# Optimization experiments

Measured on AMD Instinct MI355X. Metric: run time of the kernel, lower is better.

Reference implementation:

```python
import jax, jax.numpy as jnp
import numpy as np

N_NODES = 20000
N_EDGES = 320000
F_IN = 64      # num_node_features
C = 64         # out_features (per-head channels, concat=False)
H = 4          # n_heads
L = 3          # n_layers (stackable since F_IN == C)
N_RES = 2
N_PAIRS = 8192
EDGE_DIM = 9
HID = 64 * C   # ResNetGated hidden dim = 64 * out_features
N_EXPERTS = 8


def setup_inputs() -> dict:
    key = jax.random.key(0)
    ks = jax.random.split(key, 24)
    s = 0.05
    f32 = jnp.float32
    inp = {}
    inp["x"] = jax.random.normal(ks[0], (N_NODES, F_IN), f32)
    inp["edge_index"] = jax.random.randint(ks[1], (2, N_EDGES), 0, N_NODES)
    inp["edge_attr"] = jax.random.normal(ks[2], (N_EDGES, EDGE_DIM), f32)
    inp["edge_cross"] = jax.random.randint(ks[3], (N_PAIRS, 2), 0, N_NODES)
    inp["types"] = jax.random.randint(ks[4], (N_PAIRS,), 0, N_EXPERTS)
    # GATv2 encoder params, stacked over L layers (layer 0 in-dim == C)
    inp["gat_Wl"] = jax.random.normal(ks[5], (L, F_IN, H * C), f32) * s
    inp["gat_bl"] = jnp.full((L, H * C), 0.01, f32)
    inp["gat_Wr"] = jax.random.normal(ks[6], (L, F_IN, H * C), f32) * s
    inp["gat_br"] = jnp.full((L, H * C), 0.01, f32)
    inp["gat_We"] = jax.random.normal(ks[7], (L, EDGE_DIM, H * C), f32) * s  # lin_edge, no bias
    inp["gat_att"] = jax.random.normal(ks[8], (L, H, C), f32) * s
    inp["gat_bias"] = jnp.zeros((L, C), f32)
    inp["gat_gates"] = jax.random.normal(ks[9], (L,), f32) * 0.5
    # 8 type-routed experts: ResNetGated(2C -> 64C -> 2C) x N_RES, then Linear(2C, 1)
    inp["res_W1"] = jax.random.normal(ks[10], (N_EXPERTS, N_RES, 2 * C, HID), f32) * s
    inp["res_b1"] = jnp.full((N_EXPERTS, N_RES, HID), 0.01, f32)
    inp["res_W2"] = jax.random.normal(ks[11], (N_EXPERTS, N_RES, HID, 2 * C), f32) * s
    inp["res_b2"] = jnp.full((N_EXPERTS, N_RES, 2 * C), 0.01, f32)
    inp["res_gates"] = jax.random.normal(ks[12], (N_EXPERTS, N_RES), f32) * 0.5
    inp["head_W"] = jax.random.normal(ks[13], (N_EXPERTS, 2 * C, 1), f32) * s
    inp["head_b"] = jnp.full((N_EXPERTS, 1), 0.01, f32)
    return inp


def _gat_layer(h, src, tgt, ea, Wl, bl, Wr, br, We, att, bias):
    # GATv2Conv with edge features, concat=False (mean over heads)
    n = h.shape[0]
    nh, c = att.shape
    xl = (h @ Wl + bl).reshape(n, nh, c)   # source transform (x_j)
    xr = (h @ Wr + br).reshape(n, nh, c)   # target transform (x_i)
    e = (ea @ We).reshape(-1, nh, c)
    m = jax.nn.leaky_relu(xl[src] + xr[tgt] + e, 0.2)       # [E,H,C]
    logits = jnp.einsum('ehc,hc->eh', m, att)               # [E,H]
    mx = jax.ops.segment_max(logits, tgt, num_segments=n)
    a = jnp.exp(logits - mx[tgt])
    den = jax.ops.segment_sum(a, tgt, num_segments=n)
    alpha = a / den[tgt]                                     # segment softmax over in-edges
    out = jax.ops.segment_sum(xl[src] * alpha[:, :, None], tgt, num_segments=n)
    return out.mean(axis=1) + bias


def reference(x, edge_index, edge_attr, edge_cross, types,
              gat_Wl, gat_bl, gat_Wr, gat_br, gat_We, gat_att, gat_bias, gat_gates,
              res_W1, res_b1, res_W2, res_b2, res_gates, head_W, head_b):
    src, tgt = edge_index[0], edge_index[1]
    g = jax.nn.sigmoid(gat_gates)
    h = _gat_layer(x, src, tgt, edge_attr, gat_Wl[0], gat_bl[0], gat_Wr[0], gat_br[0],
                   gat_We[0], gat_att[0], gat_bias[0])
    for i in range(1, gat_Wl.shape[0]):
        h = jax.nn.leaky_relu(h, 0.01)
        hi = _gat_layer(h, src, tgt, edge_attr, gat_Wl[i], gat_bl[i], gat_Wr[i], gat_br[i],
                        gat_We[i], gat_att[i], gat_bias[i])
        h = g[i - 1] * hi + (1 - g[i - 1]) * h
    # pair gather + feature interleave: x[edge_cross].transpose(1,2).reshape(P, 2C)
    pair = h[edge_cross]                               # [P,2,C]
    p = pair.shape[0]
    z0 = jnp.swapaxes(pair, 1, 2).reshape(p, -1)        # [P,2C]
    outs = []
    for e in range(res_W1.shape[0]):
        z = z0
        ge = jax.nn.sigmoid(res_gates[e])
        for r in range(res_W1.shape[1]):
            z = jax.nn.relu(z)
            y = jax.nn.relu(z @ res_W1[e, r] + res_b1[e, r]) @ res_W2[e, r] + res_b2[e, r]
            z = ge[r] * y + (1 - ge[r]) * z
        outs.append(z @ head_W[e] + head_b[e])          # [P,1]
    all_out = jnp.stack(outs)                           # [8,P,1]
    per_row = all_out[types, jnp.arange(p)]             # [P,1] per-row expert output
    order = jnp.argsort(types, stable=True)             # concat groups type 0..7, stable in-group
    return per_row[order]
```

## Files before the change

### kernel.cpp

```cpp
#include <hip/hip_runtime.h>

#define NN 20000
#define NE 320000
#define NL 3
#define NP 8192
#define EDIM 9
#define TROWS 32
#define MAXT 272
#define CAPR (MAXT*TROWS)
#define NB ((NN+255)/256)

typedef _Float16 f16x8 __attribute__((ext_vector_type(8)));
typedef float f32x4 __attribute__((ext_vector_type(4)));

#define GLL16(g,l) __builtin_amdgcn_global_load_lds((const __attribute__((address_space(1))) unsigned int*)(g), (__attribute__((address_space(3))) unsigned int*)(l), 16, 0, 0)

__device__ __forceinline__ float sigm(float x){ return 1.f/(1.f+__expf(-x)); }

__device__ __forceinline__ float dpp_sum64(float x){
  x += __int_as_float(__builtin_amdgcn_update_dpp(0, __float_as_int(x), 0x111, 0xf, 0xf, true));
  x += __int_as_float(__builtin_amdgcn_update_dpp(0, __float_as_int(x), 0x112, 0xf, 0xf, true));
  x += __int_as_float(__builtin_amdgcn_update_dpp(0, __float_as_int(x), 0x114, 0xf, 0xf, true));
  x += __int_as_float(__builtin_amdgcn_update_dpp(0, __float_as_int(x), 0x118, 0xf, 0xf, true));
  x += __int_as_float(__builtin_amdgcn_update_dpp(0, __float_as_int(x), 0x142, 0xf, 0xf, true));
  x += __int_as_float(__builtin_amdgcn_update_dpp(0, __float_as_int(x), 0x143, 0xf, 0xf, true));
  return __uint_as_float(__builtin_amdgcn_readlane(__float_as_uint(x), 63));
}

__global__ void k_deg(const int* __restrict__ ei, int* __restrict__ deg){
  int e=blockIdx.x*blockDim.x+threadIdx.x; if(e<NE) atomicAdd(&deg[ei[NE+e]],1);
}

__global__ __launch_bounds__(256) void k_scan1(const int* __restrict__ deg, int* __restrict__ incl, int* __restrict__ bsum){
  __shared__ int sh[256];
  int b=blockIdx.x, tid=threadIdx.x;
  int i=b*256+tid;
  int v=(i<NN)?deg[i]:0;
  sh[tid]=v; __syncthreads();
  for(int o=1;o<256;o<<=1){
    int t=(tid>=o)?sh[tid-o]:0; __syncthreads();
    sh[tid]+=t; __syncthreads();
  }
  if(i<NN) incl[i]=sh[tid];
  if(tid==255) bsum[b]=sh[255];
}
__global__ __launch_bounds__(256) void k_scan3(const int* __restrict__ deg, const int* __restrict__ incl,
                        const int* __restrict__ bsum, int* __restrict__ row_ptr, int* __restrict__ cursor){
  __shared__ int sh[256];
  int b=blockIdx.x, tid=threadIdx.x;
  sh[tid]=(tid<b && tid<NB)?bsum[tid]:0;
  __syncthreads();
  for(int o=128;o>0;o>>=1){ if(tid<o) sh[tid]+=sh[tid+o]; __syncthreads(); }
  int boff=sh[0];
  int i=b*256+tid;
  if(i<NN){
    int r=incl[i]+boff;
    row_ptr[i+1]=r; cursor[i]=r-deg[i];
  }
  if(i==0) row_ptr[0]=0;
}

__global__ void k_fill_csr2(const int* __restrict__ ei, const float* __restrict__ ea,
    int* __restrict__ cursor, int* __restrict__ csr_src, float* __restrict__ eas){
  int e=blockIdx.x*blockDim.x+threadIdx.x;
  if(e<NE){
    int t=ei[NE+e]; int pos=atomicAdd(&cursor[t],1);
    csr_src[pos]=ei[e];
    const float* s=ea+(size_t)e*9;
    float* d=eas+(size_t)pos*12;
    #pragma unroll
    for(int k=0;k<9;++k) d[k]=s[k];
    d[9]=0.f; d[10]=0.f; d[11]=0.f;
  }
}

__global__ __launch_bounds__(256) void k_sort(const int* __restrict__ types, int* __restrict__ meta,
    int* __restrict__ slotp, int* __restrict__ islot){
  __shared__ int cnt[256][8];
  __shared__ int tot[8];
  __shared__ int base_s[8], pad_s[8];
  int tid=threadIdx.x;
  int lc[8]={0,0,0,0,0,0,0,0};
  int tl[32];
  for(int i=0;i<32;++i){ int ty=types[tid*32+i]; tl[i]=ty; lc[ty]++; }
  #pragma unroll
  for(int t=0;t<8;++t) cnt[tid][t]=lc[t];
  __syncthreads();
  if(tid<8){
    int run=0;
    for(int j=0;j<256;++j){ int v=cnt[j][tid]; cnt[j][tid]=run; run+=v; }
    tot[tid]=run;
  }
  __syncthreads();
  if(tid==0){
    int b=0, pb=0, nt=0;
    for(int t=0;t<8;++t){
      base_s[t]=b; pad_s[t]=pb;
      meta[t]=tot[t]; meta[8+t]=b; meta[16+t]=pb;
      int ntt=(tot[t]+31)>>5;
      for(int j=0;j<ntt;++j){ meta[32+nt]=t; meta[32+MAXT+nt]=pb+j*32; nt++; }
      b+=tot[t]; pb+=ntt*32;
    }
    meta[24]=nt; meta[25]=pb;
  }
  __syncthreads();
  if(tid<8){
    int t=tid; int ntt=(tot[t]+31)>>5;
    for(int sr=tot[t]; sr<ntt*32; ++sr) islot[pad_s[t]+sr]=-1;
  }
  int run[8];
  #pragma unroll
  for(int t=0;t<8;++t) run[t]=cnt[tid][t];
  for(int i=0;i<32;++i){
    int p=tid*32+i; int t=tl[i]; int r=run[t]++;
    int pos=base_s[t]+r, slot=pad_s[t]+r;
    slotp[p]=slot; islot[slot]=pos;
  }
}

__global__ __launch_bounds__(256) void k_nodexf(const float* __restrict__ hin,
    const float* __restrict__ Wl, const float* __restrict__ bl,
    const float* __restrict__ Wr, const float* __restrict__ br,
    float* __restrict__ xl, float* __restrict__ xr, int lk){
  __shared__ float hsT[64][68];
  __shared__ float ws[64][68];
  int bid=blockIdx.x;
  int n0=(bid>>3)*64, ch=bid&7;
  const float* W=(ch<4)?Wl:Wr;
  const float* bb=(ch<4)?bl:br;
  float* outp=(ch<4)?xl:xr;
  int c0=(ch&3)*64;
  int tid=threadIdx.x;

  for(int idx=tid; idx<64*16; idx+=256){
    int r=idx&63, kq=idx>>6;
    int n=n0+r;
    float4 v=make_float4(0.f,0.f,0.f,0.f);
    if(n<NN) v=*(const float4*)&hin[(size_t)n*64+kq*4];
    if(lk){
      v.x=v.x>0.f?v.x:0.01f*v.x; v.y=v.y>0.f?v.y:0.01f*v.y;
      v.z=v.z>0.f?v.z:0.01f*v.z; v.w=v.w>0.f?v.w:0.01f*v.w;
    }
    hsT[kq*4+0][r]=v.x; hsT[kq*4+1][r]=v.y; hsT[kq*4+2][r]=v.z; hsT[kq*4+3][r]=v.w;
  }
  for(int idx=tid; idx<64*16; idx+=256){
    int k=idx>>4, j4=idx&15;
    *(float4*)&ws[k][j4*4]=*(const float4*)&W[(size_t)k*256+c0+j4*4];
  }
  __syncthreads();

  int ty=tid>>4, tx=tid&15;
  float acc[4][4]={};
  #pragma unroll 4
  for(int k=0;k<64;++k){
    float4 a=*(const float4*)&hsT[k][4*ty];
    float4 b=*(const float4*)&ws[k][4*tx];
    float aa[4]={a.x,a.y,a.z,a.w}, bbv[4]={b.x,b.y,b.z,b.w};
    #pragma unroll
    for(int i=0;i<4;++i){
      #pragma unroll
      for(int j=0;j<4;++j) acc[i][j]=fmaf(aa[i],bbv[j],acc[i][j]);
    }
  }
  float4 bias4=*(const float4*)&bb[c0+4*tx];
  #pragma unroll
  for(int i=0;i<4;++i){
    int n=n0+4*ty+i;
    if(n<NN){
      float4 o=make_float4(acc[i][0]+bias4.x, acc[i][1]+bias4.y, acc[i][2]+bias4.z, acc[i][3]+bias4.w);
      *(float4*)&outp[(size_t)n*256+c0+4*tx]=o;
    }
  }
}

__global__ __launch_bounds__(256) void k_agg2(const float* __restrict__ xl, const float* __restrict__ xr,
    const float* __restrict__ eas, const int* __restrict__ csr_src, const int* __restrict__ row_ptr,
    const float* __restrict__ WeL, const float* __restrict__ attL,
    const float* __restrict__ biasL, const float* __restrict__ gates, int layer,
    const float* __restrict__ hprev, float* __restrict__ hout){
  __shared__ float red[4][64];
  int n=blockIdx.x, tid=threadIdx.x;
  float w0=WeL[tid],      w1=WeL[256+tid],  w2=WeL[512+tid],  w3=WeL[768+tid],  w4=WeL[1024+tid];
  float w5=WeL[1280+tid], w6=WeL[1536+tid], w7=WeL[1792+tid], w8=WeL[2048+tid];
  float att_t=attL[tid];
  float xr_t=xr[(size_t)n*256+tid];
  int s=row_ptr[n], t=row_ptr[n+1];
  float den=0.f, acc=0.f;

  auto body=[&](float xlv, int j){
    const float4* ep=(const float4*)(eas+(size_t)j*12);
    float4 e0=ep[0], e1=ep[1];
    float e8=eas[(size_t)j*12+8];
    float ev=e0.x*w0+e0.y*w1+e0.z*w2+e0.w*w3+e1.x*w4+e1.y*w5+e1.z*w6+e1.w*w7+e8*w8;
    float m=xlv+xr_t+ev;
    m=m>0.f?m:0.2f*m;
    float pt=dpp_sum64(m*att_t);
    float a=__expf(pt);
    den+=a; acc+=a*xlv;
  };

  float x0=0.f,x1=0.f,x2=0.f,x3=0.f;
  if(s+0<t) x0=xl[(size_t)csr_src[s+0]*256+tid];
  if(s+1<t) x1=xl[(size_t)csr_src[s+1]*256+tid];
  if(s+2<t) x2=xl[(size_t)csr_src[s+2]*256+tid];
  if(s+3<t) x3=xl[(size_t)csr_src[s+3]*256+tid];
  int j=s;
  while(j+7<t){
    float y0=xl[(size_t)csr_src[j+4]*256+tid];
    float y1=xl[(size_t)csr_src[j+5]*256+tid];
    float y2=xl[(size_t)csr_src[j+6]*256+tid];
    float y3=xl[(size_t)csr_src[j+7]*256+tid];
    body(x0,j); body(x1,j+1); body(x2,j+2); body(x3,j+3);
    x0=y0; x1=y1; x2=y2; x3=y3;
    j+=4;
  }
  if(j<t){ body(x0,j); ++j; }
  if(j<t){ body(x1,j); ++j; }
  if(j<t){ body(x2,j); ++j; }
  if(j<t){ body(x3,j); ++j; }
  while(j<t){ body(xl[(size_t)csr_src[j]*256+tid], j); ++j; }

  float rdn=den>0.f?1.f/den:0.f;
  int h=tid>>6, cc=tid&63;
  red[h][cc]=acc*rdn;
  __syncthreads();
  if(tid<64){
    float mean=(red[0][tid]+red[1][tid]+red[2][tid]+red[3][tid])*0.25f + biasL[tid];
    float o;
    if(layer==0) o=mean;
    else{
      float hp=hprev[(size_t)n*64+tid];
      hp=hp>0.f?hp:0.01f*hp;
      float g=sigm(gates[layer-1]);
      o=g*mean+(1.f-g)*hp;
    }
    hout[(size_t)n*64+tid]=o;
  }
}

__global__ __launch_bounds__(256) void k_prep_all(const float* __restrict__ rW1, _Float16* __restrict__ w1t,
    const float* __restrict__ rW2, _Float16* __restrict__ w2t,
    const float* __restrict__ hfin, const int* __restrict__ ecross,
    const int* __restrict__ slotp, float* __restrict__ z){
  __shared__ float lds[128*33];
  int bigbid=blockIdx.x, tid=threadIdx.x;
  if(bigbid<2048){
    int bid=bigbid, er=bid>>7, ch=bid&127;
    const float* s=rW1+(size_t)er*128*4096 + ch*32;
    for(int idx=tid; idx<128*32; idx+=256){ int k=idx>>5, jl=idx&31; lds[k*33+jl]=s[(size_t)k*4096+jl]; }
    __syncthreads();
    _Float16* d=w1t+(size_t)bid*4096;
    for(int g=tid; g<512; g+=256){
      int jl=g>>4, k8=g&15;
      f16x8 v;
      #pragma unroll
      for(int t=0;t<8;++t) v[t]=(_Float16)lds[(k8*8+t)*33+jl];
      int elem=(jl*128+k8*8)^((jl&7)<<3);
      *(f16x8*)(&d[elem])=v;
    }
  }else if(bigbid<4096){
    int bid=bigbid-2048, er=bid>>7, ch=bid&127;
    const float* s=rW2+(size_t)er*4096*128 + (size_t)ch*32*128;
    for(int idx=tid; idx<32*128; idx+=256){ int j=idx>>7, n=idx&127; lds[j*130+n]=s[(size_t)j*128+n]; }
    __syncthreads();
    _Float16* d=w2t+(size_t)bid*4096;
    for(int g=tid; g<512; g+=256){
      int n=g>>2, j8=g&3;
      f16x8 v;
      #pragma unroll
      for(int t=0;t<8;++t) v[t]=(_Float16)lds[(j8*8+t)*130+n];
      int elem=(n*32+j8*8)^((n&7)<<3);
      *(f16x8*)(&d[elem])=v;
    }
  }else{
    int g=(bigbid-4096)*256+tid;
    int p=g>>6, c=g&63;
    int a=ecross[2*p], b=ecross[2*p+1];
    int slot=slotp[p];
    float2 v; v.x=hfin[(size_t)a*64+c]; v.y=hfin[(size_t)b*64+c];
    ((float2*)(z+(size_t)slot*128))[c]=v;
  }
}

__global__ __launch_bounds__(256) void k_resmfma(const float* __restrict__ zin,
    const _Float16* __restrict__ w1t, const _Float16* __restrict__ w2t,
    const float* __restrict__ b1all, const int* __restrict__ meta,
    float* __restrict__ ypart, int rb)
{
  __shared__ _Float16 zh[32*128];
  __shared__ _Float16 wb[3][8192];
  __shared__ _Float16 ts[2][32*32];
  __shared__ float b1s[1024];
  int bidl=blockIdx.x;
  int bid=(bidl&7)*132+(bidl>>3);
  int v=bid>>2, hq=bid&3;
  int nt=meta[24];
  if(v>=nt) return;
  int e=meta[32+v], row0=meta[32+MAXT+v];
  int er=e*2+rb;
  const _Float16* w1b=w1t+(size_t)er*524288 + (size_t)hq*32*4096;
  const _Float16* w2b=w2t+(size_t)er*524288 + (size_t)hq*32*4096;
  const float* b1g=b1all+(size_t)er*4096 + hq*1024;
  int tid=threadIdx.x, l=tid&63, w=tid>>6;
  int lm=l&15, lq=l>>4;
  int s16=(w&1)*16, jh=w>>1;
  int arow=s16+lm;

  for(int g=tid; g<512; g+=256){
    int row=g>>4, slot=g&15;
    const float* src=zin+(size_t)(row0+row)*128+slot*8;
    float4 v0=*(const float4*)src;
    float4 v1=*(const float4*)(src+4);
    f16x8 hv;
    hv[0]=(_Float16)fmaxf(v0.x,0.f); hv[1]=(_Float16)fmaxf(v0.y,0.f);
    hv[2]=(_Float16)fmaxf(v0.z,0.f); hv[3]=(_Float16)fmaxf(v0.w,0.f);
    hv[4]=(_Float16)fmaxf(v1.x,0.f); hv[5]=(_Float16)fmaxf(v1.y,0.f);
    hv[6]=(_Float16)fmaxf(v1.z,0.f); hv[7]=(_Float16)fmaxf(v1.w,0.f);
    *(f16x8*)(&zh[(row*128+slot*8)^((row&7)<<3)])=hv;
  }
  for(int g=tid; g<1024; g+=256) b1s[g]=b1g[g];

  #pragma unroll
  for(int s=0;s<2;++s){
    int so=(w*2+s)*512;
    GLL16(w1b+so+l*8, &wb[0][so]);
    GLL16(w2b+so+l*8, &wb[0][4096+so]);
  }
  {
    const _Float16* g1=w1b+4096;
    const _Float16* g2=w2b+4096;
    #pragma unroll
    for(int s=0;s<2;++s){
      int so=(w*2+s)*512;
      GLL16(g1+so+l*8, &wb[1][so]);
      GLL16(g2+so+l*8, &wb[1][4096+so]);
    }
  }
  asm volatile("s_waitcnt lgkmcnt(0)" ::: "memory");
  __builtin_amdgcn_sched_barrier(0);
  __builtin_amdgcn_s_barrier();

  f32x4 yacc[4];
  #pragma unroll
  for(int i=0;i<4;++i){ yacc[i][0]=0.f; yacc[i][1]=0.f; yacc[i][2]=0.f; yacc[i][3]=0.f; }

  int buf=0, tb=2;
  for(int cc=0; cc<32; ++cc){
    if(cc<31){ asm volatile("s_waitcnt vmcnt(4)" ::: "memory"); }
    else     { asm volatile("s_waitcnt vmcnt(0)" ::: "memory"); }
    __builtin_amdgcn_sched_barrier(0);
    __builtin_amdgcn_s_barrier();
    if(cc<30){
      const _Float16* g1=w1b+(size_t)(cc+2)*4096;
      const _Float16* g2=w2b+(size_t)(cc+2)*4096;
      #pragma unroll
      for(int s=0;s<2;++s){
        int so=(w*2+s)*512;
        GLL16(g1+so+l*8, &wb[tb][so]);
        GLL16(g2+so+l*8, &wb[tb][4096+so]);
      }
    }

    f32x4 tacc={0.f,0.f,0.f,0.f};
    int j=jh*16+lm;
    #pragma unroll
    for(int ks=0;ks<4;++ks){
      f16x8 a=*(const f16x8*)(&zh[(arow*128+ks*32+lq*8)^((arow&7)<<3)]);
      f16x8 b=*(const f16x8*)(&wb[buf][(j*128+ks*32+lq*8)^((j&7)<<3)]);
      tacc=__builtin_amdgcn_mfma_f32_16x16x32_f16(a,b,tacc,0,0,0);
    }
    float b1v=b1s[cc*32+j];
    int tbuf=cc&1;
    #pragma unroll
    for(int r=0;r<4;++r){
      int trow=s16+lq*4+r;
      ts[tbuf][(trow*32+j)^((trow&7)<<3)]=(_Float16)fmaxf(tacc[r]+b1v,0.f);
    }
    asm volatile("s_waitcnt lgkmcnt(0)" ::: "memory");
    __builtin_amdgcn_sched_barrier(0);
    __builtin_amdgcn_s_barrier();

    f16x8 a2=*(const f16x8*)(&ts[tbuf][(arow*32+lq*8)^((arow&7)<<3)]);
    #pragma unroll
    for(int nf=0;nf<4;++nf){
      int n=jh*64+nf*16+lm;
      f16x8 b=*(const f16x8*)(&wb[buf][4096+((n*32+lq*8)^((n&7)<<3))]);
      yacc[nf]=__builtin_amdgcn_mfma_f32_16x16x32_f16(a2,b,yacc[nf],0,0,0);
    }
    buf=(buf==2)?0:buf+1;
    tb =(tb ==2)?0:tb +1;
  }

  float* yp=ypart+(size_t)hq*CAPR*128;
  #pragma unroll
  for(int nf=0;nf<4;++nf){
    int col=jh*64+nf*16+lm;
    #pragma unroll
    for(int r=0;r<4;++r)
      yp[(size_t)(row0+s16+lq*4+r)*128+col]=yacc[nf][r];
  }
}

__global__ __launch_bounds__(256) void k_comb(const float* __restrict__ zin, const float* __restrict__ ypart,
    const float* __restrict__ b2all, const float* __restrict__ gates, const int* __restrict__ meta,
    int rb, float* __restrict__ zout,
    const float* __restrict__ hWg, const float* __restrict__ hbg, const int* __restrict__ islot,
    float* __restrict__ out)
{
  int v=blockIdx.x;
  if(v>=meta[24]) return;
  int e=meta[32+v], row0=meta[32+MAXT+v];
  int er=e*2+rb;
  float ge=sigm(gates[er]);
  const float* b2=b2all+(size_t)er*128;
  int tid=threadIdx.x;
  const size_t HS=(size_t)CAPR*128;
  if(rb==0){
    for(int idx=tid; idx<32*128; idx+=256){
      int r=idx>>7, c=idx&127;
      size_t o=(size_t)(row0+r)*128+c;
      float y=ypart[o]+ypart[HS+o]+ypart[2*HS+o]+ypart[3*HS+o];
      float zr=fmaxf(zin[o],0.f);
      zout[o]=ge*(y+b2[c])+(1.f-ge)*zr;
    }
  }else{
    int r=tid>>3, cs=tid&7;
    float acc=0.f;
    size_t ro=(size_t)(row0+r)*128;
    #pragma unroll
    for(int q=0;q<16;++q){
      int c=cs*16+q;
      size_t o=ro+c;
      float y=ypart[o]+ypart[HS+o]+ypart[2*HS+o]+ypart[3*HS+o];
      float zr=fmaxf(zin[o],0.f);
      float zf=ge*(y+b2[c])+(1.f-ge)*zr;
      acc+=zf*hWg[e*128+c];
    }
    acc+=__shfl_xor(acc,1); acc+=__shfl_xor(acc,2); acc+=__shfl_xor(acc,4);
    if(cs==0){
      int pos=islot[row0+r];
      if(pos>=0) out[pos]=acc+hbg[e];
    }
  }
}

extern "C" void kernel_launch(void* const* d_in, const int* in_sizes, int n_in,
                              void* d_out, int out_size, void* d_ws, size_t ws_size,
                              hipStream_t stream){
  const float* x     =(const float*)d_in[0];
  const int*   ei    =(const int*)  d_in[1];
  const float* ea    =(const float*)d_in[2];
  const int*   ecross=(const int*)  d_in[3];
  const int*   types =(const int*)  d_in[4];
  const float* gWl   =(const float*)d_in[5];
  const float* gbl   =(const float*)d_in[6];
  const float* gWr   =(const float*)d_in[7];
  const float* gbr   =(const float*)d_in[8];
  const float* gWe   =(const float*)d_in[9];
  const float* gatt  =(const float*)d_in[10];
  const float* gbias =(const float*)d_in[11];
  const float* ggate =(const float*)d_in[12];
  const float* rW1   =(const float*)d_in[13];
  const float* rb1   =(const float*)d_in[14];
  const float* rW2   =(const float*)d_in[15];
  const float* rb2   =(const float*)d_in[16];
  const float* rg    =(const float*)d_in[17];
  const float* hW    =(const float*)d_in[18];
  const float* hb    =(const float*)d_in[19];
  float* out=(float*)d_out;

  char* base=(char*)d_ws;
  size_t off=0;
  auto alloc=[&](size_t bytes)->char*{
    char* p=base+off;
    off=(off+bytes+511)&~((size_t)511);
    return p;
  };
  float* hA     =(float*)alloc((size_t)NN*64*4);
  float* hB     =(float*)alloc((size_t)NN*64*4);
  int*   deg    =(int*)  alloc((size_t)NN*4);
  int*   row_ptr=(int*)  alloc((size_t)(NN+1)*4);
  int*   cursor =(int*)  alloc((size_t)NN*4);
  int*   incl   =(int*)  alloc((size_t)NN*4);
  int*   bsum   =(int*)  alloc(256*4);
  int*   csr_src=(int*)  alloc((size_t)(NE+16)*4);
  int*   meta   =(int*)  alloc(1024*4);
  int*   slotp  =(int*)  alloc((size_t)NP*4);
  int*   islot  =(int*)  alloc((size_t)CAPR*4);
  float* zA     =(float*)alloc((size_t)CAPR*128*4);
  size_t uoff=off;
  float* xl =(float*)(base+uoff);
  float* xr =(float*)(base+uoff+(size_t)NN*256*4);
  float* eas=(float*)(base+uoff+(size_t)NN*256*4*2);
  _Float16* w1t=(_Float16*)(base+uoff);
  _Float16* w2t=(_Float16*)(base+uoff+(size_t)16*524288*2);
  float* ypart =(float*)(base+uoff+(size_t)16*524288*2*2);
  size_t gat_bytes=(size_t)NN*256*4*2 + (size_t)(NE*12+16)*4;
  size_t exp_bytes=(size_t)16*524288*2*2 + (size_t)4*CAPR*128*4;
  size_t need=uoff+(gat_bytes>exp_bytes?gat_bytes:exp_bytes);
  if(ws_size<need) return;
  float* zB=hB;

  hipMemsetAsync(deg,0,(size_t)NN*4,stream);
  k_deg<<<(NE+255)/256,256,0,stream>>>(ei,deg);
  k_scan1<<<NB,256,0,stream>>>(deg,incl,bsum);
  k_scan3<<<NB,256,0,stream>>>(deg,incl,bsum,row_ptr,cursor);
  k_fill_csr2<<<(NE+255)/256,256,0,stream>>>(ei,ea,cursor,csr_src,eas);
  k_sort<<<1,256,0,stream>>>(types,meta,slotp,islot);

  const float* hcur=x;
  float* hnext=hA;
  for(int L=0;L<NL;++L){
    k_nodexf<<<((NN+63)/64)*8,256,0,stream>>>(hcur, gWl+(size_t)L*64*256, gbl+(size_t)L*256,
                                              gWr+(size_t)L*64*256, gbr+(size_t)L*256, xl, xr, L>0?1:0);
    k_agg2<<<NN,256,0,stream>>>(xl,xr,eas,csr_src,row_ptr, gWe+(size_t)L*EDIM*256,
                                gatt+(size_t)L*256, gbias+(size_t)L*64, ggate, L, hcur, hnext);
    hcur=hnext;
    hnext=(hcur==hA)?hB:hA;
  }

  k_prep_all<<<6144,256,0,stream>>>(rW1,w1t,rW2,w2t,hcur,ecross,slotp,zA);

  k_resmfma<<<1056,256,0,stream>>>(zA,w1t,w2t,rb1,meta,ypart,0);
  k_comb<<<MAXT,256,0,stream>>>(zA,ypart,rb2,rg,meta,0,zB,hW,hb,islot,out);
  k_resmfma<<<1056,256,0,stream>>>(zB,w1t,w2t,rb1,meta,ypart,1);
  k_comb<<<MAXT,256,0,stream>>>(zB,ypart,rb2,rg,meta,1,zA,hW,hb,islot,out);

  (void)in_sizes; (void)n_in; (void)out_size;
}
```

Measured before the change: 573.9 us.

## Keep A operand in registers and shrink weight pipeline to double buffering

Drops the shared-memory z tile and loads each wave's A fragments for the first GEMM straight into registers once, with relu and fp16 conversion applied on load. Cuts the weight staging ring from three buffers to two, which lowers LDS use per block to about 38KB and may allow more resident blocks per CU. The cost is a shallower prefetch: each step now waits for all outstanding loads (vmcnt 0) before computing, so weight-load latency is less hidden.

```diff
diff --git a/kernel.cpp b/kernel.cpp
--- a/kernel.cpp
+++ b/kernel.cpp
@@ -287,8 +287,7 @@
     const float* __restrict__ b1all, const int* __restrict__ meta,
     float* __restrict__ ypart, int rb)
 {
-  __shared__ _Float16 zh[32*128];
-  __shared__ _Float16 wb[3][8192];
+  __shared__ _Float16 wb[2][8192];
   __shared__ _Float16 ts[2][32*32];
   __shared__ float b1s[1024];
   int bidl=blockIdx.x;
@@ -306,17 +305,21 @@
   int s16=(w&1)*16, jh=w>>1;
   int arow=s16+lm;
 
-  for(int g=tid; g<512; g+=256){
-    int row=g>>4, slot=g&15;
-    const float* src=zin+(size_t)(row0+row)*128+slot*8;
-    float4 v0=*(const float4*)src;
-    float4 v1=*(const float4*)(src+4);
-    f16x8 hv;
-    hv[0]=(_Float16)fmaxf(v0.x,0.f); hv[1]=(_Float16)fmaxf(v0.y,0.f);
-    hv[2]=(_Float16)fmaxf(v0.z,0.f); hv[3]=(_Float16)fmaxf(v0.w,0.f);
-    hv[4]=(_Float16)fmaxf(v1.x,0.f); hv[5]=(_Float16)fmaxf(v1.y,0.f);
-    hv[6]=(_Float16)fmaxf(v1.z,0.f); hv[7]=(_Float16)fmaxf(v1.w,0.f);
-    *(f16x8*)(&zh[(row*128+slot*8)^((row&7)<<3)])=hv;
+  f16x8 af[4];
+  {
+    const float* zr=zin+(size_t)(row0+arow)*128;
+    #pragma unroll
+    for(int ks=0;ks<4;++ks){
+      const float* src=zr+ks*32+lq*8;
+      float4 v0=*(const float4*)src;
+      float4 v1=*(const float4*)(src+4);
+      f16x8 hv;
+      hv[0]=(_Float16)fmaxf(v0.x,0.f); hv[1]=(_Float16)fmaxf(v0.y,0.f);
+      hv[2]=(_Float16)fmaxf(v0.z,0.f); hv[3]=(_Float16)fmaxf(v0.w,0.f);
+      hv[4]=(_Float16)fmaxf(v1.x,0.f); hv[5]=(_Float16)fmaxf(v1.y,0.f);
+      hv[6]=(_Float16)fmaxf(v1.z,0.f); hv[7]=(_Float16)fmaxf(v1.w,0.f);
+      af[ks]=hv;
+    }
   }
   for(int g=tid; g<1024; g+=256) b1s[g]=b1g[g];
 
@@ -326,16 +329,6 @@
     GLL16(w1b+so+l*8, &wb[0][so]);
     GLL16(w2b+so+l*8, &wb[0][4096+so]);
   }
-  {
-    const _Float16* g1=w1b+4096;
-    const _Float16* g2=w2b+4096;
-    #pragma unroll
-    for(int s=0;s<2;++s){
-      int so=(w*2+s)*512;
-      GLL16(g1+so+l*8, &wb[1][so]);
-      GLL16(g2+so+l*8, &wb[1][4096+so]);
-    }
-  }
   asm volatile("s_waitcnt lgkmcnt(0)" ::: "memory");
   __builtin_amdgcn_sched_barrier(0);
   __builtin_amdgcn_s_barrier();
@@ -344,20 +337,20 @@
   #pragma unroll
   for(int i=0;i<4;++i){ yacc[i][0]=0.f; yacc[i][1]=0.f; yacc[i][2]=0.f; yacc[i][3]=0.f; }
 
-  int buf=0, tb=2;
   for(int cc=0; cc<32; ++cc){
-    if(cc<31){ asm volatile("s_waitcnt vmcnt(4)" ::: "memory"); }
-    else     { asm volatile("s_waitcnt vmcnt(0)" ::: "memory"); }
+    int buf=cc&1;
+    asm volatile("s_waitcnt vmcnt(0)" ::: "memory");
     __builtin_amdgcn_sched_barrier(0);
     __builtin_amdgcn_s_barrier();
-    if(cc<30){
-      const _Float16* g1=w1b+(size_t)(cc+2)*4096;
-      const _Float16* g2=w2b+(size_t)(cc+2)*4096;
+    if(cc<31){
+      const _Float16* g1=w1b+(size_t)(cc+1)*4096;
+      const _Float16* g2=w2b+(size_t)(cc+1)*4096;
+      int nb=buf^1;
       #pragma unroll
       for(int s=0;s<2;++s){
         int so=(w*2+s)*512;
-        GLL16(g1+so+l*8, &wb[tb][so]);
-        GLL16(g2+so+l*8, &wb[tb][4096+so]);
+        GLL16(g1+so+l*8, &wb[nb][so]);
+        GLL16(g2+so+l*8, &wb[nb][4096+so]);
       }
     }
 
@@ -365,9 +358,8 @@
     int j=jh*16+lm;
     #pragma unroll
     for(int ks=0;ks<4;++ks){
-      f16x8 a=*(const f16x8*)(&zh[(arow*128+ks*32+lq*8)^((arow&7)<<3)]);
       f16x8 b=*(const f16x8*)(&wb[buf][(j*128+ks*32+lq*8)^((j&7)<<3)]);
-      tacc=__builtin_amdgcn_mfma_f32_16x16x32_f16(a,b,tacc,0,0,0);
+      tacc=__builtin_amdgcn_mfma_f32_16x16x32_f16(af[ks],b,tacc,0,0,0);
     }
     float b1v=b1s[cc*32+j];
     int tbuf=cc&1;
@@ -387,8 +379,6 @@
       f16x8 b=*(const f16x8*)(&wb[buf][4096+((n*32+lq*8)^((n&7)<<3))]);
       yacc[nf]=__builtin_amdgcn_mfma_f32_16x16x32_f16(a2,b,yacc[nf],0,0,0);
     }
-    buf=(buf==2)?0:buf+1;
-    tb =(tb ==2)?0:tb +1;
   }
 
   float* yp=ypart+(size_t)hq*CAPR*128;
```

After: 555.4 us. 3.2% less time.
